# Kernel optimization log

Hardware: AMD Instinct MI355X
Metric: run time of the kernel (lower is better)

The kernel has to match this reference:

```python
import jax, jax.numpy as jnp
import numpy as np

HEAD_DIM = 128
NUM_HEADS = 16
NUM_KV_HEADS = 16
ROPE_MAX_POS = 4096
ROPE_BASE = 10000.0


def _rope_tables(seq_len):
    # cos/sin cached tables: [S, D/2]
    inv_freq = 1.0 / (ROPE_BASE ** (jnp.arange(0, HEAD_DIM, 2, dtype=jnp.float32) / HEAD_DIM))
    t = jnp.arange(seq_len, dtype=jnp.float32)
    freqs = jnp.outer(t, inv_freq)
    return jnp.cos(freqs), jnp.sin(freqs)


def _apply_rope(x, cos, sin):
    # x: [B, S, H, D]; cos/sin: [S, D/2] -> broadcast over heads as [S, 1, D/2]
    orig_dtype = x.dtype
    c = cos[:, None, :]
    s = sin[:, None, :]
    xf = x.astype(jnp.float32)
    x_real, x_im = jnp.split(xf, 2, axis=-1)  # half-split (not interleaved) RoPE
    x_real_e = x_real * c - x_im * s
    x_im_e = x_im * c + x_real * s
    return jnp.concatenate((x_real_e, x_im_e), axis=-1).astype(orig_dtype)


def setup_inputs() -> dict:
    key = jax.random.key(0)
    k1, k2, k3 = jax.random.split(key, 3)
    B, S, H = 1, 4096, 2048
    hidden_states = jax.random.normal(k1, (B, S, H), dtype=jnp.float32)
    # trunc-normal-ish init, std ~ 1/sqrt(fan_in)
    w_qkv = jax.random.normal(k2, ((NUM_HEADS + 2 * NUM_KV_HEADS) * HEAD_DIM, H), dtype=jnp.float32) / jnp.sqrt(jnp.float32(H))
    w_o = jax.random.normal(k3, (H, NUM_HEADS * HEAD_DIM), dtype=jnp.float32) / jnp.sqrt(jnp.float32(NUM_HEADS * HEAD_DIM))
    return {"hidden_states": hidden_states, "w_qkv": w_qkv, "w_o": w_o}


def reference(hidden_states, w_qkv, w_o):
    B, S, _ = hidden_states.shape
    qkv = jnp.einsum('bsh,oh->bso', hidden_states, w_qkv)
    qkv = qkv.reshape(B, S, NUM_HEADS + 2 * NUM_KV_HEADS, HEAD_DIM)
    q = qkv[:, :, :NUM_HEADS]
    k = qkv[:, :, NUM_HEADS:NUM_HEADS + NUM_KV_HEADS]
    v = qkv[:, :, NUM_HEADS + NUM_KV_HEADS:]

    cos, sin = _rope_tables(S)
    q = _apply_rope(q, cos, sin)
    k = _apply_rope(k, cos, sin)

    scale = 1.0 / jnp.sqrt(jnp.float32(HEAD_DIM)).astype(q.dtype)
    # scores: [B, H, Sq, Sk]
    scores = jnp.einsum('bqhd,bkhd->bhqk', q, k) * scale
    causal = jnp.tril(jnp.ones((S, S), dtype=bool))
    scores = jnp.where(causal[None, None], scores, jnp.finfo(scores.dtype).min)
    probs = jax.nn.softmax(scores, axis=-1)
    attn = jnp.einsum('bhqk,bkhd->bqhd', probs, v)
    attn = attn.reshape(B, S, NUM_HEADS * HEAD_DIM)
    return jnp.einsum('bso,ho->bsh', attn, w_o)
```

## Files before the change

kernel.cpp:

```cpp
#include <hip/hip_runtime.h>

typedef __bf16 bf16;
typedef __bf16 bf16x8 __attribute__((ext_vector_type(8)));
typedef __bf16 bf16x4 __attribute__((ext_vector_type(4)));
typedef float f32x4 __attribute__((ext_vector_type(4)));

#define SEQ 4096
#define QKV_LD 6144
#define HNUM 16

__device__ __forceinline__ void async16(const bf16* g, bf16* l) {
    __builtin_amdgcn_global_load_lds((const __attribute__((address_space(1))) void*)g,
                                     (__attribute__((address_space(3))) void*)l, 16, 0, 0);
}

__global__ __launch_bounds__(256) void cast_f32_bf16(const float* __restrict__ src,
                                                     bf16* __restrict__ dst, int n) {
    int i = (blockIdx.x * 256 + threadIdx.x) * 8;
    if (i >= n) return;
    f32x4 a = *(const f32x4*)(src + i);
    f32x4 b = *(const f32x4*)(src + i + 4);
    bf16x8 w;
#pragma unroll
    for (int j = 0; j < 4; j++) { w[j] = (bf16)a[j]; w[4 + j] = (bf16)b[j]; }
    *(bf16x8*)(dst + i) = w;
}


__device__ __forceinline__ bf16x8 ldfrag(const bf16* slot, int row, int qd) {
    int lin  = row * 64 + qd * 16;
    int phys = lin ^ (((lin >> 9) & 1) << 5);
    return *(const bf16x8*)((const char*)slot + phys);
}

#define STAGE2(SG, SGR0, STT, SKK, SBUF, SMAT)                                  \
    {                                                                           \
        int tcl = (STT) < NT ? (STT) : NT - 1;                                  \
        const bf16* gsrc = (SG) + (size_t)(SGR0)*K + tcl * 64 + (SKK)*32;       \
        bf16* sl = &LDS[SBUF][SMAT][SKK][0];                                    \
        async16(gsrc + g0, (bf16*)((char*)sl + lb0));                           \
        async16(gsrc + g1, (bf16*)((char*)sl + lb1));                           \
    }

#define PHASE(QM, KKI, LOADB, SG, SGR0, STT, SKK, SBUF, SMAT, DOVM)             \
    {                                                                           \
        if (LOADB) {                                                            \
            _Pragma("unroll") for (int j = 0; j < 4; j++)                       \
                bB[j] = ldfrag(&LDS[bi][1][KKI][0], wc * 64 + j * 16 + ln, qd); \
        }                                                                       \
        bf16x8 aA[4];                                                           \
        _Pragma("unroll") for (int i = 0; i < 4; i++)                           \
            aA[i] = ldfrag(&LDS[bi][0][KKI][0],                                 \
                           wr * 128 + (QM)*64 + i * 16 + ln, qd);               \
        STAGE2(SG, SGR0, STT, SKK, SBUF, SMAT);                                 \
        __builtin_amdgcn_sched_barrier(0);                                      \
        if (DOVM) {                                                             \
            asm volatile("s_waitcnt vmcnt(4)" ::: "memory");                    \
            __builtin_amdgcn_sched_barrier(0);                                  \
        }                                                                       \
        __builtin_amdgcn_s_barrier();                                           \
        __builtin_amdgcn_sched_barrier(0);                                      \
        __builtin_amdgcn_s_setprio(1);                                          \
        _Pragma("unroll") for (int i = 0; i < 4; i++)                           \
            _Pragma("unroll") for (int j = 0; j < 4; j++)                       \
                acc[(QM)*4 + i][j] = __builtin_amdgcn_mfma_f32_16x16x32_bf16(   \
                    aA[i], bB[j], acc[(QM)*4 + i][j], 0, 0, 0);                 \
        __builtin_amdgcn_s_setprio(0);                                          \
        __builtin_amdgcn_sched_barrier(0);                                      \
        __builtin_amdgcn_s_barrier();                                           \
        __builtin_amdgcn_sched_barrier(0);                                      \
    }

__global__ __launch_bounds__(512, 2) void gemm256_nt(const bf16* __restrict__ A,
                                                     const bf16* __restrict__ B,
                                                     bf16* __restrict__ C,
                                                     int M, int N, int K) {
    __shared__ __align__(16) bf16 LDS[2][2][2][256 * 32];
    const int tid  = threadIdx.x;
    const int wave = tid >> 6, lane = tid & 63;
    const int qd = lane >> 4, ln = lane & 15;
    const int wr = wave >> 2, wc = wave & 3;
    const int bm = blockIdx.x * 256, bn = blockIdx.y * 256;
    const int NT = K >> 6;

    const int seg0 = wave * 2, seg1 = seg0 + 1;
    const int Pr0 = seg0 * 1024 + lane * 16;
    const int Pr1 = seg1 * 1024 + lane * 16;
    const int Lr0 = Pr0 ^ (((Pr0 >> 9) & 1) << 5);
    const int Lr1 = Pr1 ^ (((Pr1 >> 9) & 1) << 5);
    const size_t g0 = (size_t)(Lr0 >> 6) * K + ((Lr0 & 63) >> 1);
    const size_t g1 = (size_t)(Lr1 >> 6) * K + ((Lr1 & 63) >> 1);
    const int lb0 = seg0 * 1024, lb1 = seg1 * 1024;

    f32x4 acc[8][4] = {};

    STAGE2(A, bm, 0, 0, 0, 0);
    STAGE2(B, bn, 0, 0, 0, 1);
    STAGE2(A, bm, 0, 1, 0, 0);
    STAGE2(B, bn, 0, 1, 0, 1);
    STAGE2(A, bm, 1, 0, 1, 0);
    STAGE2(B, bn, 1, 0, 1, 1);
    __builtin_amdgcn_sched_barrier(0);
    asm volatile("s_waitcnt vmcnt(4)" ::: "memory");
    __builtin_amdgcn_sched_barrier(0);
    __builtin_amdgcn_s_barrier();
    __builtin_amdgcn_sched_barrier(0);

    for (int t = 0; t < NT; ++t) {
        const int bi = t & 1;
        bf16x8 bB[4];
        PHASE(0, 0, 1, A, bm, t + 1, 1, bi ^ 1, 0, 0)
        PHASE(1, 0, 0, B, bn, t + 1, 1, bi ^ 1, 1, 0)
        PHASE(0, 1, 1, A, bm, t + 2, 0, bi,     0, 0)
        PHASE(1, 1, 0, B, bn, t + 2, 0, bi,     1, 1)
    }
    asm volatile("s_waitcnt vmcnt(0)" ::: "memory");

    const size_t cb = (size_t)(bm + wr * 128 + qd * 4) * N + (bn + wc * 64 + ln);
#pragma unroll
    for (int mi = 0; mi < 8; mi++)
#pragma unroll
        for (int j = 0; j < 4; j++)
#pragma unroll
            for (int r = 0; r < 4; r++)
                C[cb + (size_t)(mi * 16 + r) * N + j * 16] = (bf16)acc[mi][j][r];
}

template <int A_F32, int B_F32, int C_F32>
__global__ __launch_bounds__(256) void gemm_nt(const void* __restrict__ Ap,
                                               const void* __restrict__ Bp,
                                               void* __restrict__ Cp,
                                               int M, int N, int K) {
    __shared__ __align__(16) bf16 sA[128 * 32];
    __shared__ __align__(16) bf16 sB[128 * 32];
    const int tid  = threadIdx.x;
    const int wave = tid >> 6, lane = tid & 63;
    const int qd = lane >> 4, ln = lane & 15;
    const int bm = blockIdx.x * 128, bn = blockIdx.y * 128;
    const int wm = (wave >> 1) * 64, wn = (wave & 1) * 64;

    const int srow = wave * 16 + (lane >> 2);
    const int scol = (lane & 3) * 8;
    const size_t rowoff = (size_t)srow * K + scol;
    const size_t rowskip = (size_t)64 * K;

    const bf16* Ab = (const bf16*)Ap + (size_t)bm * K + rowoff;
    const bf16* Bb = (const bf16*)Bp + (size_t)bn * K + rowoff;
    const float* Af = (const float*)Ap + (size_t)bm * K + rowoff;
    const float* Bf = (const float*)Bp + (size_t)bn * K + rowoff;
    bf16* sAd0 = &sA[(wave * 16) * 32];
    bf16* sAd1 = &sA[(64 + wave * 16) * 32];
    bf16* sBd0 = &sB[(wave * 16) * 32];
    bf16* sBd1 = &sB[(64 + wave * 16) * 32];
    bf16* sAw0 = &sA[srow * 32 + scol];
    bf16* sAw1 = &sA[(64 + srow) * 32 + scol];
    bf16* sBw0 = &sB[srow * 32 + scol];
    bf16* sBw1 = &sB[(64 + srow) * 32 + scol];

    f32x4 acc[4][4] = {};
    for (int k0 = 0; k0 < K; k0 += 32) {
        if (A_F32) {
            f32x4 u0 = *(const f32x4*)(Af + k0);
            f32x4 u1 = *(const f32x4*)(Af + k0 + 4);
            f32x4 u2 = *(const f32x4*)(Af + rowskip + k0);
            f32x4 u3 = *(const f32x4*)(Af + rowskip + k0 + 4);
            bf16x8 w0, w1;
#pragma unroll
            for (int i = 0; i < 4; i++) { w0[i] = (bf16)u0[i]; w0[4 + i] = (bf16)u1[i];
                                          w1[i] = (bf16)u2[i]; w1[4 + i] = (bf16)u3[i]; }
            *(bf16x8*)sAw0 = w0;
            *(bf16x8*)sAw1 = w1;
        } else {
            async16(Ab + k0, sAd0);
            async16(Ab + rowskip + k0, sAd1);
        }
        if (B_F32) {
            f32x4 u0 = *(const f32x4*)(Bf + k0);
            f32x4 u1 = *(const f32x4*)(Bf + k0 + 4);
            f32x4 u2 = *(const f32x4*)(Bf + rowskip + k0);
            f32x4 u3 = *(const f32x4*)(Bf + rowskip + k0 + 4);
            bf16x8 w0, w1;
#pragma unroll
            for (int i = 0; i < 4; i++) { w0[i] = (bf16)u0[i]; w0[4 + i] = (bf16)u1[i];
                                          w1[i] = (bf16)u2[i]; w1[4 + i] = (bf16)u3[i]; }
            *(bf16x8*)sBw0 = w0;
            *(bf16x8*)sBw1 = w1;
        } else {
            async16(Bb + k0, sBd0);
            async16(Bb + rowskip + k0, sBd1);
        }
        __syncthreads();
        bf16x8 af[4], bfr[4];
#pragma unroll
        for (int i = 0; i < 4; i++)
            af[i] = *(const bf16x8*)&sA[(wm + i * 16 + ln) * 32 + qd * 8];
#pragma unroll
        for (int j = 0; j < 4; j++)
            bfr[j] = *(const bf16x8*)&sB[(wn + j * 16 + ln) * 32 + qd * 8];
#pragma unroll
        for (int i = 0; i < 4; i++)
#pragma unroll
            for (int j = 0; j < 4; j++)
                acc[i][j] = __builtin_amdgcn_mfma_f32_16x16x32_bf16(af[i], bfr[j], acc[i][j], 0, 0, 0);
        __syncthreads();
    }
    const size_t cbase = (size_t)(bm + wm + qd * 4) * N + (bn + wn + ln);
#pragma unroll
    for (int i = 0; i < 4; i++)
#pragma unroll
        for (int j = 0; j < 4; j++)
#pragma unroll
            for (int r = 0; r < 4; r++) {
                size_t idx = cbase + (size_t)(i * 16 + r) * N + j * 16;
                if (C_F32) ((float*)Cp)[idx] = acc[i][j][r];
                else       ((bf16*)Cp)[idx] = (bf16)acc[i][j][r];
            }
}

__global__ __launch_bounds__(256) void rope_table(float* __restrict__ T) {
    int i = blockIdx.x * 256 + threadIdx.x;
    int s = i >> 6, d = i & 63;
    float inv_freq = powf(10000.0f, -(float)d * (1.0f / 64.0f));
    float ang = (float)s * inv_freq;
    T[2 * i]     = cosf(ang);
    T[2 * i + 1] = sinf(ang);
}

__global__ __launch_bounds__(256) void rope_k_tab(bf16* __restrict__ QKV,
                                                  const float* __restrict__ T) {
    const int s  = blockIdx.x;
    const int t  = threadIdx.x;
    const int hh = (blockIdx.y << 2) + (t >> 6);
    const int d  = t & 63;
    bf16* p = QKV + (size_t)s * QKV_LD + hh * 128 + d;
    float2 cs = ((const float2*)T)[(size_t)s * 64 + d];
    float x0 = (float)p[0];
    float x1 = (float)p[64];
    p[0]  = (bf16)(x0 * cs.x - x1 * cs.y);
    p[64] = (bf16)(x1 * cs.x + x0 * cs.y);
}

__global__ __launch_bounds__(256) void rope_k_inline(bf16* __restrict__ QKV) {
    const int s  = blockIdx.x;
    const int t  = threadIdx.x;
    const int hh = (blockIdx.y << 2) + (t >> 6);
    const int d  = t & 63;
    bf16* p = QKV + (size_t)s * QKV_LD + hh * 128 + d;
    float x0 = (float)p[0];
    float x1 = (float)p[64];
    float inv_freq = powf(10000.0f, -(float)d * (1.0f / 64.0f));
    float ang = (float)s * inv_freq;
    float c = cosf(ang), sn = sinf(ang);
    p[0]  = (bf16)(x0 * c - x1 * sn);
    p[64] = (bf16)(x1 * c + x0 * sn);
}

__global__ __launch_bounds__(256) void transpose_v(const bf16* __restrict__ QKV,
                                                   bf16* __restrict__ VT) {
    __shared__ bf16 t[64][65];
    const int s0 = blockIdx.x * 64;
    const int d0 = blockIdx.y * 64;
    const int r = threadIdx.x >> 3, c = threadIdx.x & 7;
#pragma unroll
    for (int u = 0; u < 2; u++) {
        bf16x8 v = *(const bf16x8*)(QKV + (size_t)(s0 + u * 32 + r) * QKV_LD + 4096 + d0 + c * 8);
#pragma unroll
        for (int e = 0; e < 8; e++) t[u * 32 + r][c * 8 + e] = v[e];
    }
    __syncthreads();
#pragma unroll
    for (int u = 0; u < 2; u++) {
        bf16x8 w;
#pragma unroll
        for (int e = 0; e < 8; e++) w[e] = t[c * 8 + e][u * 32 + r];
        *(bf16x8*)(VT + (size_t)(d0 + u * 32 + r) * SEQ + s0 + c * 8) = w;
    }
}

template <int USE_VT>
__global__ __launch_bounds__(256, 2) void flash_attn(const bf16* __restrict__ QKV,
                                                     const bf16* __restrict__ VT,
                                                     bf16* __restrict__ O) {
    __shared__ __align__(16) bf16 sK[64 * 128];
    __shared__ __align__(16) bf16 sV[128 * 64];
    __shared__ __align__(16) bf16 sP[4][32 * 64];
    const int tid  = threadIdx.x;
    const int wave = tid >> 6, lane = tid & 63;
    const int qd = lane >> 4, ln = lane & 15;
    const int h  = blockIdx.x;
    const int qtile = 31 - blockIdx.y;
    const int qw0 = qtile * 128 + wave * 32;
    const int nkv = 2 * qtile + 2;
    const float scale = 0.08838834764831843f;

    bf16x8 Qf[2][4];
#pragma unroll
    for (int qt = 0; qt < 2; qt++) {
        const bf16* Qg = QKV + (size_t)(qw0 + qt * 16 + ln) * QKV_LD + h * 128;
#pragma unroll
        for (int ks = 0; ks < 4; ks++) {
            bf16x8 q8 = *(const bf16x8*)(Qg + ks * 32 + qd * 8);
#pragma unroll
            for (int e = 0; e < 8; e++) q8[e] = (bf16)((float)q8[e] * scale);
            Qf[qt][ks] = q8;
        }
    }

    f32x4 Oacc[2][8] = {};
    float l_i[2] = {0.0f, 0.0f};

    const int krow = tid >> 4;
    const int kblk = tid & 15;
    const int vrow = tid >> 3;
    const int vblk = tid & 7;
    const int vd   = tid & 127;
    const int vh   = tid >> 7;
    const bf16* Kg  = QKV + 2048 + h * 128;
    const bf16* Vg  = QKV + 4096 + h * 128;
    const bf16* VTg = VT + (size_t)h * 128 * SEQ;

    bf16x8 Kpre[4], Vpre[4];
#pragma unroll
    for (int rr = 0; rr < 4; rr++)
        Kpre[rr] = *(const bf16x8*)(Kg + (size_t)(rr * 16 + krow) * QKV_LD + kblk * 8);
    if (USE_VT) {
#pragma unroll
        for (int u = 0; u < 4; u++)
            Vpre[u] = *(const bf16x8*)(VTg + (size_t)(u * 32 + vrow) * SEQ + vblk * 8);
    } else {
#pragma unroll
        for (int u = 0; u < 4; u++)
#pragma unroll
            for (int j = 0; j < 8; j++)
                Vpre[u][j] = Vg[(size_t)(vh * 32 + u * 8 + j) * QKV_LD + vd];
    }

    for (int kt = 0; kt < nkv; kt++) {
        const int kbase = kt * 64;
#pragma unroll
        for (int rr = 0; rr < 4; rr++) {
            int kv = rr * 16 + krow;
            *(bf16x8*)&sK[kv * 128 + ((kblk ^ (kv & 7)) * 8)] = Kpre[rr];
        }
        if (USE_VT) {
#pragma unroll
            for (int u = 0; u < 4; u++) {
                int d = u * 32 + vrow;
                *(bf16x8*)&sV[d * 64 + ((vblk ^ (d & 7)) * 8)] = Vpre[u];
            }
        } else {
#pragma unroll
            for (int u = 0; u < 4; u++)
                *(bf16x8*)&sV[vd * 64 + (((vh * 4 + u) ^ (vd & 7)) * 8)] = Vpre[u];
        }
        __syncthreads();
        if (kt + 1 < nkv) {
            const int nb = kbase + 64;
#pragma unroll
            for (int rr = 0; rr < 4; rr++)
                Kpre[rr] = *(const bf16x8*)(Kg + (size_t)(nb + rr * 16 + krow) * QKV_LD + kblk * 8);
            if (USE_VT) {
#pragma unroll
                for (int u = 0; u < 4; u++)
                    Vpre[u] = *(const bf16x8*)(VTg + (size_t)(u * 32 + vrow) * SEQ + nb + vblk * 8);
            } else {
#pragma unroll
                for (int u = 0; u < 4; u++)
#pragma unroll
                    for (int j = 0; j < 8; j++)
                        Vpre[u][j] = Vg[(size_t)(nb + vh * 32 + u * 8 + j) * QKV_LD + vd];
            }
        }
        if (kbase <= qw0 + 31) {
            f32x4 Sacc[2][4] = {};
#pragma unroll
            for (int ks = 0; ks < 4; ks++)
#pragma unroll
                for (int j = 0; j < 4; j++) {
                    bf16x8 af = *(const bf16x8*)&sK[(j * 16 + ln) * 128 + (((ks * 4 + qd) ^ (ln & 7)) * 8)];
                    Sacc[0][j] = __builtin_amdgcn_mfma_f32_16x16x32_bf16(af, Qf[0][ks], Sacc[0][j], 0, 0, 0);
                    Sacc[1][j] = __builtin_amdgcn_mfma_f32_16x16x32_bf16(af, Qf[1][ks], Sacc[1][j], 0, 0, 0);
                }
#pragma unroll
            for (int qt = 0; qt < 2; qt++) {
                const int qs = qw0 + qt * 16;
                if (kbase + 63 > qs) {
#pragma unroll
                    for (int j = 0; j < 4; j++)
#pragma unroll
                        for (int r = 0; r < 4; r++)
                            if (kbase + j * 16 + qd * 4 + r > qs + ln) Sacc[qt][j][r] = -1e30f;
                }
                float psum = 0.0f;
#pragma unroll
                for (int j = 0; j < 4; j++) {
                    bf16x4 p4;
#pragma unroll
                    for (int r = 0; r < 4; r++) {
                        float p = __expf(Sacc[qt][j][r]);
                        psum += p;
                        p4[r] = (bf16)p;
                    }
                    int blk = (j * 2 + (qd >> 1)) ^ (ln & 7);
                    *(bf16x4*)&sP[wave][(qt * 16 + ln) * 64 + blk * 8 + (qd & 1) * 4] = p4;
                }
                psum += __shfl_xor(psum, 16);
                psum += __shfl_xor(psum, 32);
                l_i[qt] += psum;
            }
#pragma unroll
            for (int ks = 0; ks < 2; ks++) {
                bf16x8 pf0 = *(const bf16x8*)&sP[wave][(0 * 16 + ln) * 64 + (((ks * 4 + qd) ^ (ln & 7)) * 8)];
                bf16x8 pf1 = *(const bf16x8*)&sP[wave][(1 * 16 + ln) * 64 + (((ks * 4 + qd) ^ (ln & 7)) * 8)];
#pragma unroll
                for (int dt = 0; dt < 8; dt++) {
                    bf16x8 vf = *(const bf16x8*)&sV[(dt * 16 + ln) * 64 + (((ks * 4 + qd) ^ (ln & 7)) * 8)];
                    Oacc[0][dt] = __builtin_amdgcn_mfma_f32_16x16x32_bf16(pf0, vf, Oacc[0][dt], 0, 0, 0);
                    Oacc[1][dt] = __builtin_amdgcn_mfma_f32_16x16x32_bf16(pf1, vf, Oacc[1][dt], 0, 0, 0);
                }
            }
        }
        __syncthreads();
    }
#pragma unroll
    for (int qt = 0; qt < 2; qt++) {
        float linv[4];
#pragma unroll
        for (int r = 0; r < 4; r++)
            linv[r] = 1.0f / __shfl(l_i[qt], (lane & 48) | (qd * 4 + r));
        bf16* Ob = O + (size_t)(qw0 + qt * 16 + qd * 4) * 2048 + h * 128 + ln;
#pragma unroll
        for (int dt = 0; dt < 8; dt++)
#pragma unroll
            for (int r = 0; r < 4; r++)
                Ob[(size_t)r * 2048 + dt * 16] = (bf16)(Oacc[qt][dt][r] * linv[r]);
    }
}

extern "C" void kernel_launch(void* const* d_in, const int* in_sizes, int n_in,
                              void* d_out, int out_size, void* d_ws, size_t ws_size,
                              hipStream_t stream) {
    const float* X    = (const float*)d_in[0];
    const float* Wqkv = (const float*)d_in[1];
    const float* Wo   = (const float*)d_in[2];
    float* out = (float*)d_out;
    bf16* QKV = (bf16*)d_ws;
    bf16* ATT = QKV + (size_t)4096 * 6144;

    const size_t nX = (size_t)4096 * 2048, nWq = (size_t)6144 * 2048, nWo = (size_t)2048 * 2048;
    const size_t need = (nX * 3 + nWq * 2 + nWo) * 2 + nX * 2;

    if (ws_size >= need) {
        bf16* Xb  = ATT + nX;
        bf16* Wqb = Xb + nX;
        bf16* Wob = Wqb + nWq;
        bf16*  VT  = Xb;
        float* Tab = (float*)Wqb;
        cast_f32_bf16<<<(int)(nX  / 8 / 256), 256, 0, stream>>>(X, Xb, (int)nX);
        cast_f32_bf16<<<(int)(nWq / 8 / 256), 256, 0, stream>>>(Wqkv, Wqb, (int)nWq);
        cast_f32_bf16<<<(int)(nWo / 8 / 256), 256, 0, stream>>>(Wo, Wob, (int)nWo);
        gemm256_nt<<<dim3(16, 24), 512, 0, stream>>>(Xb, Wqb, QKV, 4096, 6144, 2048);
        rope_table<<<1024, 256, 0, stream>>>(Tab);
        rope_k_tab<<<dim3(4096, 8), 256, 0, stream>>>(QKV, Tab);
        transpose_v<<<dim3(64, 32), 256, 0, stream>>>(QKV, VT);
        flash_attn<1><<<dim3(HNUM, 32), 256, 0, stream>>>(QKV, VT, ATT);
        gemm_nt<0, 0, 1><<<dim3(32, 16), 256, 0, stream>>>(ATT, Wob, out, 4096, 2048, 2048);
    } else {
        gemm_nt<1, 1, 0><<<dim3(32, 48), 256, 0, stream>>>(X, Wqkv, QKV, 4096, 6144, 2048);
        rope_k_inline<<<dim3(4096, 8), 256, 0, stream>>>(QKV);
        flash_attn<0><<<dim3(HNUM, 32), 256, 0, stream>>>(QKV, (const bf16*)nullptr, ATT);
        gemm_nt<0, 1, 1><<<dim3(32, 16), 256, 0, stream>>>(ATT, Wo, out, 4096, 2048, 2048);
    }
}
```

Baseline: 440.9 us.

## Merge prep kernels, fuse RoPE with V transpose, reorder attention q-tiles

Folds the three f32-to-bf16 casts and the RoPE table build into one prep launch, and merges the RoPE application and the V transpose into one launch. The RoPE path is also vectorized to 8 elements per thread. The table now lives in the ATT buffer instead of Wqb, because Wqb is overwritten in the same launch and would be clobbered. Flash attention now pairs heavy q-tiles with light ones in the grid order to balance causal work, which cuts launch overhead and small-kernel tails.

```diff
diff --git a/kernel.cpp b/kernel.cpp
--- a/kernel.cpp
+++ b/kernel.cpp
@@ -14,18 +14,34 @@
                                      (__attribute__((address_space(3))) void*)l, 16, 0, 0);
 }
 
-__global__ __launch_bounds__(256) void cast_f32_bf16(const float* __restrict__ src,
-                                                     bf16* __restrict__ dst, int n) {
-    int i = (blockIdx.x * 256 + threadIdx.x) * 8;
-    if (i >= n) return;
-    f32x4 a = *(const f32x4*)(src + i);
-    f32x4 b = *(const f32x4*)(src + i + 4);
-    bf16x8 w;
-#pragma unroll
-    for (int j = 0; j < 4; j++) { w[j] = (bf16)a[j]; w[4 + j] = (bf16)b[j]; }
-    *(bf16x8*)(dst + i) = w;
-}
-
+__global__ __launch_bounds__(256) void prep(const float* __restrict__ X, bf16* __restrict__ Xb,
+                                            const float* __restrict__ Wq, bf16* __restrict__ Wqb,
+                                            const float* __restrict__ Wo, bf16* __restrict__ Wob,
+                                            float* __restrict__ T) {
+    const int b = blockIdx.x, t = threadIdx.x;
+    if (b < 12288) {
+        const float* src;
+        bf16* dst;
+        int off;
+        if (b < 4096)       { src = X;  dst = Xb;  off = b; }
+        else if (b < 10240) { src = Wq; dst = Wqb; off = b - 4096; }
+        else                { src = Wo; dst = Wob; off = b - 10240; }
+        int i = (off * 256 + t) * 8;
+        f32x4 a = *(const f32x4*)(src + i);
+        f32x4 c = *(const f32x4*)(src + i + 4);
+        bf16x8 w;
+#pragma unroll
+        for (int j = 0; j < 4; j++) { w[j] = (bf16)a[j]; w[4 + j] = (bf16)c[j]; }
+        *(bf16x8*)(dst + i) = w;
+    } else {
+        int i = (b - 12288) * 256 + t;
+        int s = i >> 6, d = i & 63;
+        float inv_freq = powf(10000.0f, -(float)d * (1.0f / 64.0f));
+        float ang = (float)s * inv_freq;
+        T[2 * i]     = cosf(ang);
+        T[2 * i + 1] = sinf(ang);
+    }
+}
 
 __device__ __forceinline__ bf16x8 ldfrag(const bf16* slot, int row, int qd) {
     int lin  = row * 64 + qd * 16;
@@ -217,27 +233,49 @@
             }
 }
 
-__global__ __launch_bounds__(256) void rope_table(float* __restrict__ T) {
-    int i = blockIdx.x * 256 + threadIdx.x;
-    int s = i >> 6, d = i & 63;
-    float inv_freq = powf(10000.0f, -(float)d * (1.0f / 64.0f));
-    float ang = (float)s * inv_freq;
-    T[2 * i]     = cosf(ang);
-    T[2 * i + 1] = sinf(ang);
-}
-
-__global__ __launch_bounds__(256) void rope_k_tab(bf16* __restrict__ QKV,
-                                                  const float* __restrict__ T) {
-    const int s  = blockIdx.x;
-    const int t  = threadIdx.x;
-    const int hh = (blockIdx.y << 2) + (t >> 6);
-    const int d  = t & 63;
-    bf16* p = QKV + (size_t)s * QKV_LD + hh * 128 + d;
-    float2 cs = ((const float2*)T)[(size_t)s * 64 + d];
-    float x0 = (float)p[0];
-    float x1 = (float)p[64];
-    p[0]  = (bf16)(x0 * cs.x - x1 * cs.y);
-    p[64] = (bf16)(x1 * cs.x + x0 * cs.y);
+__global__ __launch_bounds__(256) void rope_tv(bf16* __restrict__ QKV,
+                                               const float* __restrict__ T,
+                                               bf16* __restrict__ VT) {
+    __shared__ bf16 tl[64][65];
+    const int b = blockIdx.x, t = threadIdx.x;
+    if (b < 4096) {
+        const int s  = b;
+        const int hh = t >> 3;
+        const int d0 = (t & 7) * 8;
+        bf16* p = QKV + (size_t)s * QKV_LD + hh * 128 + d0;
+        bf16x8 x0 = *(const bf16x8*)(p);
+        bf16x8 x1 = *(const bf16x8*)(p + 64);
+        const float2* Tb = (const float2*)T + (size_t)s * 64 + d0;
+        bf16x8 y0, y1;
+#pragma unroll
+        for (int e = 0; e < 8; e++) {
+            float2 cs = Tb[e];
+            float a = (float)x0[e], c = (float)x1[e];
+            y0[e] = (bf16)(a * cs.x - c * cs.y);
+            y1[e] = (bf16)(c * cs.x + a * cs.y);
+        }
+        *(bf16x8*)(p)      = y0;
+        *(bf16x8*)(p + 64) = y1;
+    } else {
+        const int b2 = b - 4096;
+        const int s0 = (b2 & 63) * 64;
+        const int d0 = (b2 >> 6) * 64;
+        const int r = t >> 3, c = t & 7;
+#pragma unroll
+        for (int u = 0; u < 2; u++) {
+            bf16x8 v = *(const bf16x8*)(QKV + (size_t)(s0 + u * 32 + r) * QKV_LD + 4096 + d0 + c * 8);
+#pragma unroll
+            for (int e = 0; e < 8; e++) tl[u * 32 + r][c * 8 + e] = v[e];
+        }
+        __syncthreads();
+#pragma unroll
+        for (int u = 0; u < 2; u++) {
+            bf16x8 w;
+#pragma unroll
+            for (int e = 0; e < 8; e++) w[e] = tl[c * 8 + e][u * 32 + r];
+            *(bf16x8*)(VT + (size_t)(d0 + u * 32 + r) * SEQ + s0 + c * 8) = w;
+        }
+    }
 }
 
 __global__ __launch_bounds__(256) void rope_k_inline(bf16* __restrict__ QKV) {
@@ -255,28 +293,6 @@
     p[64] = (bf16)(x1 * c + x0 * sn);
 }
 
-__global__ __launch_bounds__(256) void transpose_v(const bf16* __restrict__ QKV,
-                                                   bf16* __restrict__ VT) {
-    __shared__ bf16 t[64][65];
-    const int s0 = blockIdx.x * 64;
-    const int d0 = blockIdx.y * 64;
-    const int r = threadIdx.x >> 3, c = threadIdx.x & 7;
-#pragma unroll
-    for (int u = 0; u < 2; u++) {
-        bf16x8 v = *(const bf16x8*)(QKV + (size_t)(s0 + u * 32 + r) * QKV_LD + 4096 + d0 + c * 8);
-#pragma unroll
-        for (int e = 0; e < 8; e++) t[u * 32 + r][c * 8 + e] = v[e];
-    }
-    __syncthreads();
-#pragma unroll
-    for (int u = 0; u < 2; u++) {
-        bf16x8 w;
-#pragma unroll
-        for (int e = 0; e < 8; e++) w[e] = t[c * 8 + e][u * 32 + r];
-        *(bf16x8*)(VT + (size_t)(d0 + u * 32 + r) * SEQ + s0 + c * 8) = w;
-    }
-}
-
 template <int USE_VT>
 __global__ __launch_bounds__(256, 2) void flash_attn(const bf16* __restrict__ QKV,
                                                      const bf16* __restrict__ VT,
@@ -288,7 +304,8 @@
     const int wave = tid >> 6, lane = tid & 63;
     const int qd = lane >> 4, ln = lane & 15;
     const int h  = blockIdx.x;
-    const int qtile = 31 - blockIdx.y;
+    const int y  = blockIdx.y;
+    const int qtile = (y < 16) ? (31 - y) : (y - 16);
     const int qw0 = qtile * 128 + wave * 32;
     const int nkv = 2 * qtile + 2;
     const float scale = 0.08838834764831843f;
@@ -455,14 +472,10 @@
         bf16* Wqb = Xb + nX;
         bf16* Wob = Wqb + nWq;
         bf16*  VT  = Xb;
-        float* Tab = (float*)Wqb;
-        cast_f32_bf16<<<(int)(nX  / 8 / 256), 256, 0, stream>>>(X, Xb, (int)nX);
-        cast_f32_bf16<<<(int)(nWq / 8 / 256), 256, 0, stream>>>(Wqkv, Wqb, (int)nWq);
-        cast_f32_bf16<<<(int)(nWo / 8 / 256), 256, 0, stream>>>(Wo, Wob, (int)nWo);
+        float* Tab = (float*)ATT;
+        prep<<<13312, 256, 0, stream>>>(X, Xb, Wqkv, Wqb, Wo, Wob, Tab);
         gemm256_nt<<<dim3(16, 24), 512, 0, stream>>>(Xb, Wqb, QKV, 4096, 6144, 2048);
-        rope_table<<<1024, 256, 0, stream>>>(Tab);
-        rope_k_tab<<<dim3(4096, 8), 256, 0, stream>>>(QKV, Tab);
-        transpose_v<<<dim3(64, 32), 256, 0, stream>>>(QKV, VT);
+        rope_tv<<<6144, 256, 0, stream>>>(QKV, Tab, VT);
         flash_attn<1><<<dim3(HNUM, 32), 256, 0, stream>>>(QKV, VT, ATT);
         gemm_nt<0, 0, 1><<<dim3(32, 16), 256, 0, stream>>>(ATT, Wob, out, 4096, 2048, 2048);
     } else {
```

Result: faster. 430.4 us (-2.4%).
